# Kernel tuning notes

Measured on AMD Instinct MI355X. Metric: run time of the kernel, lower is better.

## Reference

```python
import jax, jax.numpy as jnp
import numpy as np

jax.config.update("jax_enable_x64", True)  # Q16.16 int64 fixed-point arithmetic requires 64-bit ints

F = 16                 # FixedPointConfig.COMPUTE_FRAC_BITS (Q16.16)
ONE = 1 << F

B, S, D_IN, D_OUT = 2, 2048, 4096, 4096


def setup_inputs() -> dict:
    key = jax.random.key(0)
    k1, k2 = jax.random.split(key)
    x = jax.random.normal(k1, (B, S, D_IN), dtype=jnp.float32)
    weight = jax.random.normal(k2, (D_OUT, D_IN), dtype=jnp.float32)
    return {"x": x, "weight": weight}


def _to_fixed(x):
    # to_fixed_point: float -> Q16.16 int64
    return jnp.round(x * ONE).astype(jnp.int64)


def _activation_quant_fixed(xf):
    # per-token 8-bit quant/dequant, all in Q16.16 integer arithmetic
    max_vals = jnp.max(jnp.abs(xf), axis=-1, keepdims=True)
    min_val = int(1e-5 * ONE)  # == 0 at frac_bits=16 (faithful to source)
    max_vals = jnp.maximum(max_vals, min_val)
    target_max = 127 << F
    # fixed_div(target_max, max_vals, F, F, F): (a << F) // b
    scale = (target_max << F) // max_vals
    # fixed_mul(x, scale, F, F, F): (a*b) >> F  (arithmetic shift == floor-div)
    x_scaled = (xf * scale) >> F
    x_clamped = jnp.clip(x_scaled, -(128 << F), 127 << F)
    # fixed_reciprocal(scale, F, F): (1 << 2F) // scale
    scale_inv = (1 << (2 * F)) // scale
    return (x_clamped * scale_inv) >> F


def reference(x, weight):
    # --- quantize_weights() ---
    wf = _to_fixed(weight)                                   # Q16.16
    mean_abs = jnp.sum(jnp.abs(wf)) // wf.size               # fixed_mean (Q16.16 scalar)
    # fixed_div(wf, mean_abs, F, F, 0) -> integer-valued; round+clamp to {-1,0,1}
    w_ternary = jnp.clip(wf // mean_abs, -1, 1).astype(jnp.int8)

    # --- forward ---
    xq = _activation_quant_fixed(_to_fixed(x))               # [B,S,D] Q16.16 int64
    xq2 = xq.reshape(-1, D_IN)
    # Ternary GEMM replacing the per-output-feature masked-sum loop.
    # |xq| <= 128<<16 ~ 8.4e6 and K=4096 => |acc| <= 3.4e10 < 2^53, so a
    acc = jnp.dot(xq2.astype(jnp.float64), w_ternary.astype(jnp.float64).T)
    out = jnp.round(acc).astype(jnp.int64)
    out = out.astype(jnp.int32).astype(jnp.int64)            # replicate torch .to(int32) wrap
    scale_inv = (1 << (2 * F)) // mean_abs                   # fixed_reciprocal of weight_scale
    out = (out * scale_inv) >> F                             # fixed_mul dequant/rescale
    out = out.reshape(B, S, D_OUT)
    return out.astype(jnp.float32) / ONE                     # from_fixed_point
```

## Files before the change

### kernel.cpp

```cpp
#include <hip/hip_runtime.h>
#include <stdint.h>

typedef int v4i  __attribute__((ext_vector_type(4)));
typedef int v16i __attribute__((ext_vector_type(16)));

static constexpr int Mdim = 4096;
static constexpr int Ndim = 4096;
static constexpr int Kdim = 4096;

static constexpr size_t TILE_BYTES  = 128u * 4096u;
static constexpr size_t OFF_ROWPAR  = 4096;
static constexpr size_t OFF_BT      = 1u << 20;
static constexpr size_t OFF_A0      = 17u << 20;
static constexpr size_t PLANE_BYTES = 16u << 20;

__device__ __forceinline__ void gload16(const void* g, void* l) {
  __builtin_amdgcn_global_load_lds(
      (const __attribute__((address_space(1))) char*)g,
      (__attribute__((address_space(3))) char*)l, 16, 0, 0);
}

__global__ void k_wsum(const float* __restrict__ w, unsigned long long* __restrict__ ws) {
  int tid = blockIdx.x * blockDim.x + threadIdx.x;
  int stride = gridDim.x * blockDim.x;
  const float4* w4 = (const float4*)w;
  const int n4 = (Ndim * Kdim) / 4;
  unsigned long long s = 0;
  for (int i = tid; i < n4; i += stride) {
    float4 v = w4[i];
    int a = (int)rintf(v.x * 65536.f);
    int b = (int)rintf(v.y * 65536.f);
    int c = (int)rintf(v.z * 65536.f);
    int d = (int)rintf(v.w * 65536.f);
    unsigned u = (unsigned)(a < 0 ? -a : a) + (unsigned)(b < 0 ? -b : b)
               + (unsigned)(c < 0 ? -c : c) + (unsigned)(d < 0 ? -d : d);
    s += u;
  }
  #pragma unroll
  for (int off = 32; off > 0; off >>= 1) s += __shfl_down(s, off, 64);
  if ((threadIdx.x & 63) == 0) atomicAdd(ws, s);
}

__global__ void k_scalars(unsigned long long* ws) {
  unsigned long long s = ws[0];
  long long mean_abs = (long long)(s >> 24);
  if (mean_abs < 1) mean_abs = 1;
  long long siw = (long long)((1ULL << 32) / (unsigned long long)mean_abs);
  ((long long*)ws)[1] = siw;
  ((long long*)ws)[2] = mean_abs;
}

__global__ void k_tern(const float* __restrict__ w, const long long* __restrict__ scal,
                       int8_t* __restrict__ bt) {
  int t = blockIdx.x * 256 + threadIdx.x;
  int mean_abs = (int)scal[2];
  int nt = t >> 15;
  int kc = (t >> 7) & 255;
  int r  = t & 127;
  int row = nt * 128 + r;
  const float4* src = (const float4*)(w + (size_t)row * Kdim + kc * 16);
  int words[4];
  #pragma unroll
  for (int j = 0; j < 4; ++j) {
    float4 v = src[j];
    float e[4] = {v.x, v.y, v.z, v.w};
    int wrd = 0;
    #pragma unroll
    for (int q = 0; q < 4; ++q) {
      int f = (int)rintf(e[q] * 65536.f);
      int tv = (f >= mean_abs ? 1 : 0) - (f < 0 ? 1 : 0);
      wrd |= (tv & 0xff) << (8 * q);
    }
    words[j] = wrd;
  }
  *(int4*)(bt + (size_t)nt * TILE_BYTES + (size_t)kc * 2048 + (size_t)r * 16) =
      make_int4(words[0], words[1], words[2], words[3]);
}

__global__ void k_rowmax(const float* __restrict__ x, long long* __restrict__ rowpar) {
  int m = blockIdx.x;
  const float4* xr = (const float4*)(x + (size_t)m * Kdim);
  int mx = 0;
  #pragma unroll
  for (int j = 0; j < 4; ++j) {
    float4 v = xr[j * 256 + threadIdx.x];
    int a = (int)rintf(v.x * 65536.f); a = a < 0 ? -a : a; mx = a > mx ? a : mx;
    int b = (int)rintf(v.y * 65536.f); b = b < 0 ? -b : b; mx = b > mx ? b : mx;
    int c = (int)rintf(v.z * 65536.f); c = c < 0 ? -c : c; mx = c > mx ? c : mx;
    int d = (int)rintf(v.w * 65536.f); d = d < 0 ? -d : d; mx = d > mx ? d : mx;
  }
  #pragma unroll
  for (int off = 32; off > 0; off >>= 1) {
    int o = __shfl_down(mx, off, 64);
    mx = o > mx ? o : mx;
  }
  __shared__ int red[4];
  if ((threadIdx.x & 63) == 0) red[threadIdx.x >> 6] = mx;
  __syncthreads();
  if (threadIdx.x == 0) {
    int m0 = red[0];
    m0 = red[1] > m0 ? red[1] : m0;
    m0 = red[2] > m0 ? red[2] : m0;
    m0 = red[3] > m0 ? red[3] : m0;
    if (m0 < 1) m0 = 1;
    long long scale = (long long)((127ULL << 32) / (unsigned long long)m0);
    long long sinv  = (long long)((1ULL << 32) / (unsigned long long)scale);
    rowpar[2 * m]     = scale;
    rowpar[2 * m + 1] = sinv;
  }
}

__global__ void k_actq(const float* __restrict__ x, const long long* __restrict__ rowpar,
                       int8_t* __restrict__ a0, int8_t* __restrict__ a1, int8_t* __restrict__ a2) {
  int t = blockIdx.x * 256 + threadIdx.x;
  int mt = t >> 15;
  int kc = (t >> 7) & 255;
  int r  = t & 127;
  int m = mt * 128 + r;
  long long scale = rowpar[2 * m];
  long long sinv  = rowpar[2 * m + 1];
  const float4* src = (const float4*)(x + (size_t)m * Kdim + kc * 16);
  int w0[4], w1[4], w2[4];
  #pragma unroll
  for (int j = 0; j < 4; ++j) {
    float4 v = src[j];
    float e[4] = {v.x, v.y, v.z, v.w};
    int r0 = 0, r1 = 0, r2 = 0;
    #pragma unroll
    for (int q = 0; q < 4; ++q) {
      int xf = (int)rintf(e[q] * 65536.f);
      int xs = (int)(((long long)xf * scale) >> 16);
      xs = xs < -8388608 ? -8388608 : xs;
      xs = xs > 8323072 ? 8323072 : xs;
      int xq = (int)(((long long)xs * sinv) >> 16);
      int l0 = (int)(signed char)(xq & 0xff);
      int tt = (xq - l0) >> 8;
      int l1 = (int)(signed char)(tt & 0xff);
      int l2 = (tt - l1) >> 8;
      r0 |= (l0 & 0xff) << (8 * q);
      r1 |= (l1 & 0xff) << (8 * q);
      r2 |= (l2 & 0xff) << (8 * q);
    }
    w0[j] = r0; w1[j] = r1; w2[j] = r2;
  }
  size_t idx = (size_t)mt * TILE_BYTES + (size_t)kc * 2048 + (size_t)r * 16;
  *(int4*)(a0 + idx) = make_int4(w0[0], w0[1], w0[2], w0[3]);
  *(int4*)(a1 + idx) = make_int4(w1[0], w1[1], w1[2], w1[3]);
  *(int4*)(a2 + idx) = make_int4(w2[0], w2[1], w2[2], w2[3]);
}

__launch_bounds__(512)
__global__ void k_gemm(const int8_t* __restrict__ a0, const int8_t* __restrict__ a1,
                       const int8_t* __restrict__ a2, const int8_t* __restrict__ bt,
                       const long long* __restrict__ scal, float* __restrict__ out) {
  __shared__ __attribute__((aligned(16))) char lds[4][4][8192];
  int bx = blockIdx.x;
  int mt = bx >> 5;
  int nt = bx & 31;
  int tid  = threadIdx.x;
  int lane = tid & 63;
  int w    = tid >> 6;
  int wm   = w >> 1;
  int wn   = w & 1;

  const char* planes[4];
  planes[0] = (const char*)a0 + (size_t)mt * TILE_BYTES;
  planes[1] = (const char*)a1 + (size_t)mt * TILE_BYTES;
  planes[2] = (const char*)a2 + (size_t)mt * TILE_BYTES;
  planes[3] = (const char*)bt + (size_t)nt * TILE_BYTES;

  v16i acc[2][3] = {};

  auto STAGE = [&](int buf, int kt) {
    #pragma unroll
    for (int p = 0; p < 4; ++p)
      gload16(planes[p] + (size_t)kt * 8192 + (size_t)tid * 16, &lds[buf][p][tid * 16]);
  };

  auto COMPUTE = [&](int buf) {
    #pragma unroll
    for (int ks = 0; ks < 2; ++ks) {
      const int koff = (ks * 2 + (lane >> 5)) * 2048;
      v4i bfrag[2], afrag[3];
      #pragma unroll
      for (int nj = 0; nj < 2; ++nj)
        bfrag[nj] = *(const v4i*)&lds[buf][3][koff + (wn * 64 + nj * 32 + (lane & 31)) * 16];
      #pragma unroll
      for (int p = 0; p < 3; ++p)
        afrag[p] = *(const v4i*)&lds[buf][p][koff + (wm * 32 + (lane & 31)) * 16];
      __builtin_amdgcn_s_setprio(1);
      #pragma unroll
      for (int nj = 0; nj < 2; ++nj)
        #pragma unroll
        for (int p = 0; p < 3; ++p)
          acc[nj][p] = __builtin_amdgcn_mfma_i32_32x32x32_i8(afrag[p], bfrag[nj], acc[nj][p], 0, 0, 0);
      __builtin_amdgcn_s_setprio(0);
    }
  };

  const int NT = Kdim / 64;
  STAGE(0, 0); STAGE(1, 1); STAGE(2, 2);
  asm volatile("s_waitcnt vmcnt(8)" ::: "memory");
  __builtin_amdgcn_s_barrier();
  asm volatile("" ::: "memory");

  for (int t = 0; t < NT; ++t) {
    COMPUTE(t & 3);
    asm volatile("" ::: "memory");
    if (t + 3 < NT) {
      STAGE((t + 3) & 3, t + 3);
      asm volatile("s_waitcnt vmcnt(8)" ::: "memory");
    } else if (t == NT - 3) {
      asm volatile("s_waitcnt vmcnt(4)" ::: "memory");
    } else if (t == NT - 2) {
      asm volatile("s_waitcnt vmcnt(0)" ::: "memory");
    }
    if (t < NT - 1) {
      __builtin_amdgcn_s_barrier();
      asm volatile("" ::: "memory");
    }
  }

  long long siw = scal[1];
  int m0 = mt * 128 + wm * 32;
  int n0 = nt * 128 + wn * 64;
  #pragma unroll
  for (int nj = 0; nj < 2; ++nj) {
    #pragma unroll
    for (int rg = 0; rg < 16; ++rg) {
      unsigned u = (unsigned)acc[nj][0][rg]
                 + ((unsigned)acc[nj][1][rg] << 8)
                 + ((unsigned)acc[nj][2][rg] << 16);
      long long v = ((long long)(int)u * siw) >> 16;
      int row = (rg & 3) + 8 * (rg >> 2) + 4 * (lane >> 5);
      int col = nj * 32 + (lane & 31);
      out[(size_t)(m0 + row) * Ndim + (n0 + col)] = (float)v * (1.f / 65536.f);
    }
  }
}

extern "C" void kernel_launch(void* const* d_in, const int* in_sizes, int n_in,
                              void* d_out, int out_size, void* d_ws, size_t ws_size,
                              hipStream_t stream) {
  const float* x = (const float*)d_in[0];
  const float* w = (const float*)d_in[1];
  float* out = (float*)d_out;
  char* ws = (char*)d_ws;

  unsigned long long* scal = (unsigned long long*)ws;
  long long* rowpar = (long long*)(ws + OFF_ROWPAR);
  int8_t* bt = (int8_t*)(ws + OFF_BT);
  int8_t* a0 = (int8_t*)(ws + OFF_A0);
  int8_t* a1 = a0 + PLANE_BYTES;
  int8_t* a2 = a1 + PLANE_BYTES;

  hipMemsetAsync(ws, 0, 64, stream);
  k_wsum<<<1024, 256, 0, stream>>>(w, scal);
  k_scalars<<<1, 1, 0, stream>>>(scal);
  k_tern<<<4096, 256, 0, stream>>>(w, (const long long*)scal, bt);
  k_rowmax<<<4096, 256, 0, stream>>>(x, rowpar);
  k_actq<<<4096, 256, 0, stream>>>(x, rowpar, a0, a1, a2);
  k_gemm<<<1024, 512, 0, stream>>>(a0, a1, a2, bt, (const long long*)scal, out);
}
```

Measured before the change: 429.9 us.

## Fuse row-max into activation quant and enlarge GEMM tile to 128x256

Merges the row-max and activation-quantization kernels into one kernel per row, so x is read once and the row-parameter buffer round trip is dropped. The GEMM tile grows from 128x128 to 128x256, each wave computing a 64x64 block, so every staged A plane is reused across twice as many output columns. Block indices are remapped with a stride-8 swizzle, and the 4-stage pipeline with hand-placed vmcnt waits is replaced by a simpler 2-stage double buffer synchronized with __syncthreads. The shallower pipeline may expose more global-load latency, and the higher accumulator count raises register pressure.

```diff
diff --git a/kernel.cpp b/kernel.cpp
--- a/kernel.cpp
+++ b/kernel.cpp
@@ -9,7 +9,6 @@
 static constexpr int Kdim = 4096;
 
 static constexpr size_t TILE_BYTES  = 128u * 4096u;
-static constexpr size_t OFF_ROWPAR  = 4096;
 static constexpr size_t OFF_BT      = 1u << 20;
 static constexpr size_t OFF_A0      = 17u << 20;
 static constexpr size_t PLANE_BYTES = 16u << 20;
@@ -77,17 +76,24 @@
       make_int4(words[0], words[1], words[2], words[3]);
 }
 
-__global__ void k_rowmax(const float* __restrict__ x, long long* __restrict__ rowpar) {
-  int m = blockIdx.x;
-  const float4* xr = (const float4*)(x + (size_t)m * Kdim);
+__global__ void k_actq2(const float* __restrict__ x,
+                        int8_t* __restrict__ a0, int8_t* __restrict__ a1, int8_t* __restrict__ a2) {
+  int m   = blockIdx.x;
+  int tid = threadIdx.x;
+  const float4* src = (const float4*)(x + (size_t)m * Kdim + tid * 16);
+  int xf[16];
   int mx = 0;
   #pragma unroll
   for (int j = 0; j < 4; ++j) {
-    float4 v = xr[j * 256 + threadIdx.x];
-    int a = (int)rintf(v.x * 65536.f); a = a < 0 ? -a : a; mx = a > mx ? a : mx;
-    int b = (int)rintf(v.y * 65536.f); b = b < 0 ? -b : b; mx = b > mx ? b : mx;
-    int c = (int)rintf(v.z * 65536.f); c = c < 0 ? -c : c; mx = c > mx ? c : mx;
-    int d = (int)rintf(v.w * 65536.f); d = d < 0 ? -d : d; mx = d > mx ? d : mx;
+    float4 v = src[j];
+    float e[4] = {v.x, v.y, v.z, v.w};
+    #pragma unroll
+    for (int q = 0; q < 4; ++q) {
+      int f = (int)rintf(e[q] * 65536.f);
+      xf[j * 4 + q] = f;
+      int af = f < 0 ? -f : f;
+      mx = af > mx ? af : mx;
+    }
   }
   #pragma unroll
   for (int off = 32; off > 0; off >>= 1) {
@@ -95,9 +101,10 @@
     mx = o > mx ? o : mx;
   }
   __shared__ int red[4];
-  if ((threadIdx.x & 63) == 0) red[threadIdx.x >> 6] = mx;
+  __shared__ long long sc[2];
+  if ((tid & 63) == 0) red[tid >> 6] = mx;
   __syncthreads();
-  if (threadIdx.x == 0) {
+  if (tid == 0) {
     int m0 = red[0];
     m0 = red[1] > m0 ? red[1] : m0;
     m0 = red[2] > m0 ? red[2] : m0;
@@ -105,31 +112,20 @@
     if (m0 < 1) m0 = 1;
     long long scale = (long long)((127ULL << 32) / (unsigned long long)m0);
     long long sinv  = (long long)((1ULL << 32) / (unsigned long long)scale);
-    rowpar[2 * m]     = scale;
-    rowpar[2 * m + 1] = sinv;
-  }
-}
-
-__global__ void k_actq(const float* __restrict__ x, const long long* __restrict__ rowpar,
-                       int8_t* __restrict__ a0, int8_t* __restrict__ a1, int8_t* __restrict__ a2) {
-  int t = blockIdx.x * 256 + threadIdx.x;
-  int mt = t >> 15;
-  int kc = (t >> 7) & 255;
-  int r  = t & 127;
-  int m = mt * 128 + r;
-  long long scale = rowpar[2 * m];
-  long long sinv  = rowpar[2 * m + 1];
-  const float4* src = (const float4*)(x + (size_t)m * Kdim + kc * 16);
+    sc[0] = scale; sc[1] = sinv;
+  }
+  __syncthreads();
+  long long scale = sc[0];
+  long long sinv  = sc[1];
+
   int w0[4], w1[4], w2[4];
   #pragma unroll
   for (int j = 0; j < 4; ++j) {
-    float4 v = src[j];
-    float e[4] = {v.x, v.y, v.z, v.w};
     int r0 = 0, r1 = 0, r2 = 0;
     #pragma unroll
     for (int q = 0; q < 4; ++q) {
-      int xf = (int)rintf(e[q] * 65536.f);
-      int xs = (int)(((long long)xf * scale) >> 16);
+      int v  = xf[j * 4 + q];
+      int xs = (int)(((long long)v * scale) >> 16);
       xs = xs < -8388608 ? -8388608 : xs;
       xs = xs > 8323072 ? 8323072 : xs;
       int xq = (int)(((long long)xs * sinv) >> 16);
@@ -143,7 +139,7 @@
     }
     w0[j] = r0; w1[j] = r1; w2[j] = r2;
   }
-  size_t idx = (size_t)mt * TILE_BYTES + (size_t)kc * 2048 + (size_t)r * 16;
+  size_t idx = (size_t)(m >> 7) * TILE_BYTES + (size_t)tid * 2048 + (size_t)(m & 127) * 16;
   *(int4*)(a0 + idx) = make_int4(w0[0], w0[1], w0[2], w0[3]);
   *(int4*)(a1 + idx) = make_int4(w1[0], w1[1], w1[2], w1[3]);
   *(int4*)(a2 + idx) = make_int4(w2[0], w2[1], w2[2], w2[3]);
@@ -153,27 +149,28 @@
 __global__ void k_gemm(const int8_t* __restrict__ a0, const int8_t* __restrict__ a1,
                        const int8_t* __restrict__ a2, const int8_t* __restrict__ bt,
                        const long long* __restrict__ scal, float* __restrict__ out) {
-  __shared__ __attribute__((aligned(16))) char lds[4][4][8192];
-  int bx = blockIdx.x;
-  int mt = bx >> 5;
-  int nt = bx & 31;
+  __shared__ __attribute__((aligned(16))) char lds[2][5][8192];
+  int bx = (blockIdx.x & 7) * 64 + (blockIdx.x >> 3);
+  int mt = bx >> 4;
+  int nt = bx & 15;
   int tid  = threadIdx.x;
   int lane = tid & 63;
   int w    = tid >> 6;
-  int wm   = w >> 1;
-  int wn   = w & 1;
-
-  const char* planes[4];
+  int wm   = w >> 2;
+  int wn   = w & 3;
+
+  const char* planes[5];
   planes[0] = (const char*)a0 + (size_t)mt * TILE_BYTES;
   planes[1] = (const char*)a1 + (size_t)mt * TILE_BYTES;
   planes[2] = (const char*)a2 + (size_t)mt * TILE_BYTES;
-  planes[3] = (const char*)bt + (size_t)nt * TILE_BYTES;
-
-  v16i acc[2][3] = {};
+  planes[3] = (const char*)bt + (size_t)(2 * nt) * TILE_BYTES;
+  planes[4] = (const char*)bt + (size_t)(2 * nt + 1) * TILE_BYTES;
+
+  v16i acc[2][2][3] = {};
 
   auto STAGE = [&](int buf, int kt) {
     #pragma unroll
-    for (int p = 0; p < 4; ++p)
+    for (int p = 0; p < 5; ++p)
       gload16(planes[p] + (size_t)kt * 8192 + (size_t)tid * 16, &lds[buf][p][tid * 16]);
   };
 
@@ -181,60 +178,57 @@
     #pragma unroll
     for (int ks = 0; ks < 2; ++ks) {
       const int koff = (ks * 2 + (lane >> 5)) * 2048;
-      v4i bfrag[2], afrag[3];
-      #pragma unroll
-      for (int nj = 0; nj < 2; ++nj)
-        bfrag[nj] = *(const v4i*)&lds[buf][3][koff + (wn * 64 + nj * 32 + (lane & 31)) * 16];
-      #pragma unroll
-      for (int p = 0; p < 3; ++p)
-        afrag[p] = *(const v4i*)&lds[buf][p][koff + (wm * 32 + (lane & 31)) * 16];
-      __builtin_amdgcn_s_setprio(1);
-      #pragma unroll
-      for (int nj = 0; nj < 2; ++nj)
+      v4i afrag[2][3], bfrag[2];
+      #pragma unroll
+      for (int mf = 0; mf < 2; ++mf)
         #pragma unroll
         for (int p = 0; p < 3; ++p)
-          acc[nj][p] = __builtin_amdgcn_mfma_i32_32x32x32_i8(afrag[p], bfrag[nj], acc[nj][p], 0, 0, 0);
+          afrag[mf][p] = *(const v4i*)&lds[buf][p][koff + (wm * 64 + mf * 32 + (lane & 31)) * 16];
+      #pragma unroll
+      for (int nj = 0; nj < 2; ++nj) {
+        int col = wn * 64 + nj * 32 + (lane & 31);
+        bfrag[nj] = *(const v4i*)&lds[buf][3 + (col >> 7)][koff + (col & 127) * 16];
+      }
+      __builtin_amdgcn_s_setprio(1);
+      #pragma unroll
+      for (int mf = 0; mf < 2; ++mf)
+        #pragma unroll
+        for (int nj = 0; nj < 2; ++nj)
+          #pragma unroll
+          for (int p = 0; p < 3; ++p)
+            acc[mf][nj][p] = __builtin_amdgcn_mfma_i32_32x32x32_i8(
+                afrag[mf][p], bfrag[nj], acc[mf][nj][p], 0, 0, 0);
       __builtin_amdgcn_s_setprio(0);
     }
   };
 
   const int NT = Kdim / 64;
-  STAGE(0, 0); STAGE(1, 1); STAGE(2, 2);
-  asm volatile("s_waitcnt vmcnt(8)" ::: "memory");
-  __builtin_amdgcn_s_barrier();
-  asm volatile("" ::: "memory");
-
+  STAGE(0, 0);
+  __syncthreads();
   for (int t = 0; t < NT; ++t) {
-    COMPUTE(t & 3);
-    asm volatile("" ::: "memory");
-    if (t + 3 < NT) {
-      STAGE((t + 3) & 3, t + 3);
-      asm volatile("s_waitcnt vmcnt(8)" ::: "memory");
-    } else if (t == NT - 3) {
-      asm volatile("s_waitcnt vmcnt(4)" ::: "memory");
-    } else if (t == NT - 2) {
-      asm volatile("s_waitcnt vmcnt(0)" ::: "memory");
-    }
-    if (t < NT - 1) {
-      __builtin_amdgcn_s_barrier();
-      asm volatile("" ::: "memory");
-    }
+    int cur = t & 1;
+    if (t + 1 < NT) STAGE(cur ^ 1, t + 1);
+    COMPUTE(cur);
+    __syncthreads();
   }
 
   long long siw = scal[1];
-  int m0 = mt * 128 + wm * 32;
-  int n0 = nt * 128 + wn * 64;
-  #pragma unroll
-  for (int nj = 0; nj < 2; ++nj) {
-    #pragma unroll
-    for (int rg = 0; rg < 16; ++rg) {
-      unsigned u = (unsigned)acc[nj][0][rg]
-                 + ((unsigned)acc[nj][1][rg] << 8)
-                 + ((unsigned)acc[nj][2][rg] << 16);
-      long long v = ((long long)(int)u * siw) >> 16;
-      int row = (rg & 3) + 8 * (rg >> 2) + 4 * (lane >> 5);
-      int col = nj * 32 + (lane & 31);
-      out[(size_t)(m0 + row) * Ndim + (n0 + col)] = (float)v * (1.f / 65536.f);
+  #pragma unroll
+  for (int mf = 0; mf < 2; ++mf) {
+    int m0 = mt * 128 + wm * 64 + mf * 32;
+    #pragma unroll
+    for (int nj = 0; nj < 2; ++nj) {
+      int n0 = nt * 256 + wn * 64 + nj * 32;
+      #pragma unroll
+      for (int rg = 0; rg < 16; ++rg) {
+        unsigned u = (unsigned)acc[mf][nj][0][rg]
+                   + ((unsigned)acc[mf][nj][1][rg] << 8)
+                   + ((unsigned)acc[mf][nj][2][rg] << 16);
+        long long v = ((long long)(int)u * siw) >> 16;
+        int row = (rg & 3) + 8 * (rg >> 2) + 4 * (lane >> 5);
+        int col = lane & 31;
+        out[(size_t)(m0 + row) * Ndim + (n0 + col)] = (float)v * (1.f / 65536.f);
+      }
     }
   }
 }
@@ -248,7 +242,6 @@
   char* ws = (char*)d_ws;
 
   unsigned long long* scal = (unsigned long long*)ws;
-  long long* rowpar = (long long*)(ws + OFF_ROWPAR);
   int8_t* bt = (int8_t*)(ws + OFF_BT);
   int8_t* a0 = (int8_t*)(ws + OFF_A0);
   int8_t* a1 = a0 + PLANE_BYTES;
@@ -258,7 +251,6 @@
   k_wsum<<<1024, 256, 0, stream>>>(w, scal);
   k_scalars<<<1, 1, 0, stream>>>(scal);
   k_tern<<<4096, 256, 0, stream>>>(w, (const long long*)scal, bt);
-  k_rowmax<<<4096, 256, 0, stream>>>(x, rowpar);
-  k_actq<<<4096, 256, 0, stream>>>(x, rowpar, a0, a1, a2);
-  k_gemm<<<1024, 512, 0, stream>>>(a0, a1, a2, bt, (const long long*)scal, out);
-}
+  k_actq2<<<4096, 256, 0, stream>>>(x, a0, a1, a2);
+  k_gemm<<<512, 512, 0, stream>>>(a0, a1, a2, bt, (const long long*)scal, out);
+}
```

Result: no change. 430.1 us (+0.0%).
